# Optimization experiments

Measured on AMD Instinct MI355X. Metric: run time of the kernel, lower is better.

## Reference

```python
import jax, jax.numpy as jnp
import numpy as np

D_MODEL = 2048
NUM_HEADS = 16
D_KV = D_MODEL // NUM_HEADS
THETA = 10000.0
N_LORA = 4
RANK = 16
BATCH = 2
SEQ = 2048


def setup_inputs() -> dict:
    key = jax.random.key(0)
    ks = jax.random.split(key, 16)
    s = 0.02
    inp = {
        'x': jax.random.normal(ks[0], (BATCH, SEQ, D_MODEL), jnp.float32),
        'lora_start_indices': jnp.sort(jax.random.randint(ks[1], (N_LORA,), 0, BATCH)),
        'Wq': jax.random.normal(ks[2], (D_MODEL, D_MODEL), jnp.float32) * s,
        'Aq': jax.random.normal(ks[3], (N_LORA, RANK, D_MODEL), jnp.float32) * s,
        'Bq': jax.random.normal(ks[4], (N_LORA, D_MODEL, RANK), jnp.float32) * s,
        'Wk': jax.random.normal(ks[5], (D_MODEL, D_MODEL), jnp.float32) * s,
        'Ak': jax.random.normal(ks[6], (N_LORA, RANK, D_MODEL), jnp.float32) * s,
        'Bk': jax.random.normal(ks[7], (N_LORA, D_MODEL, RANK), jnp.float32) * s,
        'Wv': jax.random.normal(ks[8], (D_MODEL, D_MODEL), jnp.float32) * s,
        'Av': jax.random.normal(ks[9], (N_LORA, RANK, D_MODEL), jnp.float32) * s,
        'Bv': jax.random.normal(ks[10], (N_LORA, D_MODEL, RANK), jnp.float32) * s,
        'Wo': jax.random.normal(ks[11], (D_MODEL, D_MODEL), jnp.float32) * s,
        'Ao': jax.random.normal(ks[12], (N_LORA, RANK, D_MODEL), jnp.float32) * s,
        'Bo': jax.random.normal(ks[13], (N_LORA, D_MODEL, RANK), jnp.float32) * s,
    }
    return inp


def _adapter_ids(starts, batch):
    # each batch row b uses the adapter whose start index is the last one <= b
    ids = jnp.searchsorted(starts, jnp.arange(batch), side='right') - 1
    return jnp.clip(ids, 0, starts.shape[0] - 1)


def _multilora(x, ids, W, A, B):
    # x: [b, s, d_in]; W: [d_out, d_in]; A: [L, r, d_in]; B: [L, d_out, r]
    base = jnp.einsum('bsd,od->bso', x, W)
    Ai, Bi = A[ids], B[ids]                       # [b, r, d_in], [b, d_out, r]
    low = jnp.einsum('bsd,brd->bsr', x, Ai)
    return base + jnp.einsum('bsr,bor->bso', low, Bi)


def _rope(x):
    # x: [b, h, s, d]; interleaved pair rotation
    d = x.shape[-1]
    pos = jnp.arange(x.shape[-2], dtype=jnp.float32)
    inv_freq = THETA ** (-jnp.arange(0, d, 2, dtype=jnp.float32) / d)  # [d/2]
    ang = pos[:, None] * inv_freq[None, :]                              # [s, d/2]
    cos, sin = jnp.cos(ang), jnp.sin(ang)
    x1, x2 = x[..., 0::2], x[..., 1::2]
    o1 = x1 * cos - x2 * sin
    o2 = x1 * sin + x2 * cos
    return jnp.stack([o1, o2], axis=-1).reshape(x.shape)


def reference(x, lora_start_indices, Wq, Aq, Bq, Wk, Ak, Bk, Wv, Av, Bv, Wo, Ao, Bo):
    b, s, _ = x.shape
    ids = _adapter_ids(lora_start_indices, b)
    Q = _multilora(x, ids, Wq, Aq, Bq)
    K = _multilora(x, ids, Wk, Ak, Bk)
    V = _multilora(x, ids, Wv, Av, Bv)
    # [b, s, h*d] -> [b, h, s, d]
    split = lambda t: t.reshape(b, s, NUM_HEADS, D_KV).transpose(0, 2, 1, 3)
    Q, K, V = split(Q), split(K), split(V)
    Q, K = _rope(Q), _rope(K)
    scores = jnp.einsum('bhqd,bhkd->bhqk', Q, K) / jnp.sqrt(jnp.asarray(D_KV, x.dtype))
    causal = jnp.tril(jnp.ones((s, s), bool))
    scores = jnp.where(causal, scores, jnp.asarray(-jnp.inf, scores.dtype))
    attn = jax.nn.softmax(scores, axis=-1)
    out = jnp.einsum('bhqk,bhkd->bhqd', attn, V)
    out = out.transpose(0, 2, 1, 3).reshape(b, s, D_MODEL)
    return _multilora(out, ids, Wo, Ao, Bo)
```

## Files before the change

### kernel.cpp

```cpp
#include <hip/hip_runtime.h>

typedef unsigned short u16;
typedef unsigned int   u32;
typedef __bf16  bf16x8 __attribute__((ext_vector_type(8)));
typedef float   f32x4  __attribute__((ext_vector_type(4)));

#define D_MODEL 2048
#define SEQ     2048
#define NHEAD   16
#define DKV     128
#define RANK    16

__device__ __forceinline__ u16 f2b(float f) {
  union { float f; u32 i; } v; v.f = f;
  u32 i = v.i;
  return (u16)((i + 0x7FFFu + ((i >> 16) & 1u)) >> 16);
}
__device__ __forceinline__ u32 pack2(float lo, float hi) {
  return (u32)f2b(lo) | ((u32)f2b(hi) << 16);
}
__device__ __forceinline__ float b2f(u16 u) {
  union { u32 i; float f; } v; v.i = ((u32)u) << 16; return v.f;
}
__device__ __forceinline__ float dot2(u32 xa, u32 aa) {
  return b2f((u16)(xa & 0xFFFFu)) * b2f((u16)(aa & 0xFFFFu)) +
         b2f((u16)(xa >> 16))     * b2f((u16)(aa >> 16));
}
__device__ __forceinline__ int adapter_id(const int* starts, int b) {
  int cnt = 0;
#pragma unroll
  for (int i = 0; i < 4; ++i) cnt += (starts[i] <= b) ? 1 : 0;
  int id = cnt - 1;
  return id < 0 ? 0 : (id > 3 ? 3 : id);
}
__device__ __forceinline__ f32x4 mfma16(bf16x8 a, bf16x8 b, f32x4 c) {
  return __builtin_amdgcn_mfma_f32_16x16x32_bf16(a, b, c, 0, 0, 0);
}

struct CvtArgs {
  const float* src[13];
  u32 base[14];
};
__global__ __launch_bounds__(256) void k_convert(CvtArgs a, u16* __restrict__ dst) {
  const u32 c = blockIdx.x * 256 + threadIdx.x;
  const u32 el0 = c * 8;
  if (el0 >= a.base[13]) return;
  int t = 0;
#pragma unroll
  for (int i = 1; i < 13; ++i) t += (el0 >= a.base[i]) ? 1 : 0;
  const float* s = a.src[t] + (el0 - a.base[t]);
  const float4 lo = *(const float4*)s;
  const float4 hi = *(const float4*)(s + 4);
  uint4 r;
  r.x = pack2(lo.x, lo.y); r.y = pack2(lo.z, lo.w);
  r.z = pack2(hi.x, hi.y); r.w = pack2(hi.z, hi.w);
  *(uint4*)(dst + el0) = r;
}

template <int TAG>
__global__ __launch_bounds__(256) void k_lowrank(
    const u16* __restrict__ X, const u16* __restrict__ A0,
    const u16* __restrict__ A1, const u16* __restrict__ A2,
    const int* __restrict__ starts, float* __restrict__ low, int nout)
{
  const int m = blockIdx.x;
  const int w = threadIdx.x >> 6, lane = threadIdx.x & 63;
  const int id = adapter_id(starts, m >> 11);
  const u16* Xr = X + (size_t)m * D_MODEL;
  for (int o = w; o < nout; o += 4) {
    const int p = o >> 4, r = o & 15;
    const u16* Ar = (p == 0 ? A0 : p == 1 ? A1 : A2) + (size_t)(id * 16 + r) * D_MODEL;
    float sum = 0.f;
#pragma unroll
    for (int c = 0; c < 4; ++c) {
      const int d = c * 512 + lane * 8;
      const uint4 xv = *(const uint4*)(Xr + d);
      const uint4 av = *(const uint4*)(Ar + d);
      sum += dot2(xv.x, av.x) + dot2(xv.y, av.y) + dot2(xv.z, av.z) + dot2(xv.w, av.w);
    }
#pragma unroll
    for (int off = 32; off >= 1; off >>= 1) sum += __shfl_xor(sum, off, 64);
    if (lane == 0) low[(size_t)m * nout + o] = sum;
  }
}

template <int QKV>
__global__ __launch_bounds__(256, 2) void k_gemm(
    const u16* __restrict__ X,
    const u16* __restrict__ W0, const u16* __restrict__ W1, const u16* __restrict__ W2,
    const u16* __restrict__ B0, const u16* __restrict__ B1, const u16* __restrict__ B2,
    const float* __restrict__ low, int ldlow,
    const int* __restrict__ starts,
    u16* __restrict__ D0, u16* __restrict__ D1, u16* __restrict__ D2,
    float* __restrict__ Df)
{
  __shared__ __attribute__((aligned(16))) u16 At[128 * 32];
  __shared__ __attribute__((aligned(16))) u16 Bt[128 * 32];
  const int tid = threadIdx.x;
  const int w = tid >> 6, lane = tid & 63, quad = lane >> 4, l16 = lane & 15;
  const int wr = w >> 1, wc = w & 1;
  const int n0 = blockIdx.x * 128, m0 = blockIdx.y * 128, z = blockIdx.z;
  const u16* W  = (z == 0) ? W0 : (z == 1) ? W1 : W2;
  const u16* Bm = (z == 0) ? B0 : (z == 1) ? B1 : B2;
  u16*       D  = (z == 0) ? D0 : (z == 1) ? D1 : D2;
  const int loff = QKV ? z * RANK : 0;
  const int id = adapter_id(starts, m0 >> 11);

  const f32x4 zero4 = {0.f, 0.f, 0.f, 0.f};
  f32x4 acc[4][4];
#pragma unroll
  for (int i = 0; i < 4; ++i)
#pragma unroll
    for (int j = 0; j < 4; ++j) acc[i][j] = zero4;

  const int srow = tid >> 2;
  const int scol = (tid & 3) * 8;
  const u16* Xg = X + (size_t)(m0 + srow) * D_MODEL + scol;
  const u16* Wg = W + (size_t)(n0 + srow) * D_MODEL + scol;

  uint4 ra0 = *(const uint4*)(Xg);
  uint4 ra1 = *(const uint4*)(Xg + 64 * D_MODEL);
  uint4 rb0 = *(const uint4*)(Wg);
  uint4 rb1 = *(const uint4*)(Wg + 64 * D_MODEL);

  for (int kt = 0; kt < D_MODEL / 32; ++kt) {
    *(uint4*)(At + srow * 32 + scol)        = ra0;
    *(uint4*)(At + (64 + srow) * 32 + scol) = ra1;
    *(uint4*)(Bt + srow * 32 + scol)        = rb0;
    *(uint4*)(Bt + (64 + srow) * 32 + scol) = rb1;
    __syncthreads();
    if (kt < D_MODEL / 32 - 1) {
      const int kb = (kt + 1) * 32;
      ra0 = *(const uint4*)(Xg + kb);
      ra1 = *(const uint4*)(Xg + 64 * D_MODEL + kb);
      rb0 = *(const uint4*)(Wg + kb);
      rb1 = *(const uint4*)(Wg + 64 * D_MODEL + kb);
    }
    bf16x8 af[4], bfr[4];
#pragma unroll
    for (int i = 0; i < 4; ++i)
      af[i] = *(const bf16x8*)&At[(wr * 64 + i * 16 + l16) * 32 + quad * 8];
#pragma unroll
    for (int j = 0; j < 4; ++j)
      bfr[j] = *(const bf16x8*)&Bt[(wc * 64 + j * 16 + l16) * 32 + quad * 8];
#pragma unroll
    for (int i = 0; i < 4; ++i)
#pragma unroll
      for (int j = 0; j < 4; ++j)
        acc[i][j] = mfma16(af[i], bfr[j], acc[i][j]);
    __syncthreads();
  }

  for (int e = tid; e < 4096; e += 256) {
    const int rr = e >> 5, kk = e & 31;
    u16 av = 0, bv = 0;
    if (kk < RANK) {
      av = f2b(low[(size_t)(m0 + rr) * ldlow + loff + kk]);
      bv = Bm[((size_t)id * D_MODEL + n0 + rr) * RANK + kk];
    }
    At[rr * 32 + kk] = av;
    Bt[rr * 32 + kk] = bv;
  }
  __syncthreads();
  {
    bf16x8 af[4], bfr[4];
#pragma unroll
    for (int i = 0; i < 4; ++i)
      af[i] = *(const bf16x8*)&At[(wr * 64 + i * 16 + l16) * 32 + quad * 8];
#pragma unroll
    for (int j = 0; j < 4; ++j)
      bfr[j] = *(const bf16x8*)&Bt[(wc * 64 + j * 16 + l16) * 32 + quad * 8];
#pragma unroll
    for (int i = 0; i < 4; ++i)
#pragma unroll
      for (int j = 0; j < 4; ++j)
        acc[i][j] = mfma16(af[i], bfr[j], acc[i][j]);
  }

  if (QKV) {
    const float scale = (z == 0) ? 0.08838834764831845f : 1.0f;
    const int ropez = (z <= 1);
#pragma unroll
    for (int i = 0; i < 4; ++i) {
      const int mrow = m0 + wr * 64 + i * 16 + quad * 4;
#pragma unroll
      for (int j = 0; j < 4; ++j) {
        const int col = n0 + wc * 64 + j * 16 + l16;
        const int hh = col >> 7, jj = col & (DKV - 1);
        const float invf = exp2f(-0.20762050593046f * (float)(jj >> 1));
#pragma unroll
        for (int r = 0; r < 4; ++r) {
          const int m = mrow + r;
          const int bb = m >> 11, srw = m & (SEQ - 1);
          float v = acc[i][j][r] * scale;
          if (ropez) {
            float sn, cs;
            __sincosf((float)srw * invf, &sn, &cs);
            const float part = __shfl_xor(v, 1, 64);
            v = (jj & 1) ? (part * sn + v * cs) : (v * cs - part * sn);
          }
          D[(((size_t)(bb * NHEAD + hh)) * SEQ + srw) * DKV + jj] = f2b(v);
        }
      }
    }
  } else {
#pragma unroll
    for (int i = 0; i < 4; ++i) {
      const int mrow = m0 + wr * 64 + i * 16 + quad * 4;
#pragma unroll
      for (int j = 0; j < 4; ++j) {
        const int col = n0 + wc * 64 + j * 16 + l16;
#pragma unroll
        for (int r = 0; r < 4; ++r)
          Df[(size_t)(mrow + r) * D_MODEL + col] = acc[i][j][r];
      }
    }
  }
}

#define M0 8.0f
__global__ __launch_bounds__(256, 3) void k_flash(
    const u16* __restrict__ Q, const u16* __restrict__ K,
    const u16* __restrict__ V, u16* __restrict__ O,
    u16* __restrict__ Opart, float* __restrict__ lpart)
{
  __shared__ __attribute__((aligned(16))) u16 Kl[64 * 136];
  __shared__ __attribute__((aligned(16))) u16 VT[DKV * 72];
  __shared__ __attribute__((aligned(16))) u16 Pl[4 * 16 * 72];
  const int tid = threadIdx.x;
  const int w = tid >> 6, lane = tid & 63, quad = lane >> 4, l16 = lane & 15;
  const int cid = blockIdx.x, bh = blockIdx.y;
  const size_t base = (size_t)bh * SEQ * DKV;
  const u16* Qb = Q + base;
  const u16* Kb = K + base;
  const u16* Vb = V + base;
  const int b = bh >> 4, h = bh & 15;
  u16* Plw = &Pl[w * 1152];
  const f32x4 zero4 = {0.f, 0.f, 0.f, 0.f};

  const int dual = (cid < 16);
  const int nA   = dual ? (cid + 1) : 16;
  const int qtB  = 31 - cid;
  const int n    = dual ? 17 : 16;

  const int krr = tid >> 4;
  const int kc8 = (tid & 15) * 8;
  const int vrp = tid & 31;
  const int vcg = tid >> 5;

  int qt = cid, q0 = cid * 64;
  bf16x8 qa[4];
#pragma unroll
  for (int kc = 0; kc < 4; ++kc)
    qa[kc] = *(const bf16x8*)(Qb + (size_t)(q0 + w * 16 + l16) * DKV + kc * 32 + quad * 8);

  f32x4 oacc[8];
#pragma unroll
  for (int nn = 0; nn < 8; ++nn) oacc[nn] = zero4;
  float lr[4] = {0.f, 0.f, 0.f, 0.f};

  uint4 pk[4], pva[2], pvb[2];
#pragma unroll
  for (int it = 0; it < 4; ++it)
    pk[it] = *(const uint4*)(Kb + (size_t)(krr + it * 16) * DKV + kc8);
#pragma unroll
  for (int it = 0; it < 2; ++it) {
    pva[it] = *(const uint4*)(Vb + (size_t)(2 * vrp)     * DKV + (vcg + it * 8) * 8);
    pvb[it] = *(const uint4*)(Vb + (size_t)(2 * vrp + 1) * DKV + (vcg + it * 8) * 8);
  }

  for (int s = 0; s < n; ++s) {
    if (dual && s == nA) {
      float inv[4];
#pragma unroll
      for (int rg = 0; rg < 4; ++rg) {
        float t = lr[rg];
#pragma unroll
        for (int off = 8; off >= 1; off >>= 1) t += __shfl_xor(t, off, 64);
        inv[rg] = 1.f / t;
        lr[rg] = 0.f;
      }
#pragma unroll
      for (int nn = 0; nn < 8; ++nn) {
        const int col = h * DKV + nn * 16 + l16;
#pragma unroll
        for (int rg = 0; rg < 4; ++rg) {
          const int row = q0 + w * 16 + quad * 4 + rg;
          O[((size_t)b * SEQ + row) * D_MODEL + col] = f2b(oacc[nn][rg] * inv[rg]);
        }
#pragma unroll
        for (int e = 0; e < 4; ++e) oacc[nn][e] = 0.f;
      }
      qt = qtB; q0 = qtB * 64;
#pragma unroll
      for (int kc = 0; kc < 4; ++kc)
        qa[kc] = *(const bf16x8*)(Qb + (size_t)(q0 + w * 16 + l16) * DKV + kc * 32 + quad * 8);
    }
    const int kt = (dual && s >= nA) ? (16 + s - nA) : s;

    __syncthreads();
#pragma unroll
    for (int it = 0; it < 4; ++it)
      *(uint4*)(&Kl[(krr + it * 16) * 136 + kc8]) = pk[it];
#pragma unroll
    for (int it = 0; it < 2; ++it) {
      const int c0 = (vcg + it * 8) * 8;
      const uint4 a = pva[it], c = pvb[it];
      *(u32*)&VT[(c0 + 0) * 72 + 2 * vrp] = (a.x & 0xFFFFu) | (c.x << 16);
      *(u32*)&VT[(c0 + 1) * 72 + 2 * vrp] = (a.x >> 16)     | (c.x & 0xFFFF0000u);
      *(u32*)&VT[(c0 + 2) * 72 + 2 * vrp] = (a.y & 0xFFFFu) | (c.y << 16);
      *(u32*)&VT[(c0 + 3) * 72 + 2 * vrp] = (a.y >> 16)     | (c.y & 0xFFFF0000u);
      *(u32*)&VT[(c0 + 4) * 72 + 2 * vrp] = (a.z & 0xFFFFu) | (c.z << 16);
      *(u32*)&VT[(c0 + 5) * 72 + 2 * vrp] = (a.z >> 16)     | (c.z & 0xFFFF0000u);
      *(u32*)&VT[(c0 + 6) * 72 + 2 * vrp] = (a.w & 0xFFFFu) | (c.w << 16);
      *(u32*)&VT[(c0 + 7) * 72 + 2 * vrp] = (a.w >> 16)     | (c.w & 0xFFFF0000u);
    }
    __syncthreads();

    if (s + 1 < n) {
      const int ktn = (dual && (s + 1) >= nA) ? (16 + s + 1 - nA) : (s + 1);
      const size_t ko = (size_t)ktn * 64 * DKV;
#pragma unroll
      for (int it = 0; it < 4; ++it)
        pk[it] = *(const uint4*)(Kb + ko + (size_t)(krr + it * 16) * DKV + kc8);
#pragma unroll
      for (int it = 0; it < 2; ++it) {
        pva[it] = *(const uint4*)(Vb + ko + (size_t)(2 * vrp)     * DKV + (vcg + it * 8) * 8);
        pvb[it] = *(const uint4*)(Vb + ko + (size_t)(2 * vrp + 1) * DKV + (vcg + it * 8) * 8);
      }
    }

    f32x4 sacc[4];
#pragma unroll
    for (int jc = 0; jc < 4; ++jc) sacc[jc] = zero4;
#pragma unroll
    for (int kc = 0; kc < 4; ++kc)
#pragma unroll
      for (int jc = 0; jc < 4; ++jc) {
        const bf16x8 kb = *(const bf16x8*)&Kl[(jc * 16 + l16) * 136 + kc * 32 + quad * 8];
        sacc[jc] = mfma16(qa[kc], kb, sacc[jc]);
      }

    const int diag = (kt == qt);
#pragma unroll
    for (int rg = 0; rg < 4; ++rg) {
      const int qq = q0 + w * 16 + quad * 4 + rg;
      float psum = 0.f;
#pragma unroll
      for (int jc = 0; jc < 4; ++jc) {
        const int kk = kt * 64 + jc * 16 + l16;
        float p = __expf(sacc[jc][rg] - M0);
        if (diag && kk > qq) p = 0.f;
        psum += p;
        Plw[(quad * 4 + rg) * 72 + jc * 16 + l16] = f2b(p);
      }
      lr[rg] += psum;
    }

#pragma unroll
    for (int kc = 0; kc < 2; ++kc) {
      const bf16x8 pa = *(const bf16x8*)&Plw[l16 * 72 + kc * 32 + quad * 8];
#pragma unroll
      for (int nn = 0; nn < 8; ++nn) {
        const bf16x8 vb = *(const bf16x8*)&VT[(nn * 16 + l16) * 72 + kc * 32 + quad * 8];
        oacc[nn] = mfma16(pa, vb, oacc[nn]);
      }
    }
  }

  const int j = dual ? 1 : 0;
  const int slot = (bh * 16 + (qt - 16)) * 2 + j;
#pragma unroll
  for (int rg = 0; rg < 4; ++rg) {
#pragma unroll
    for (int off = 8; off >= 1; off >>= 1) lr[rg] += __shfl_xor(lr[rg], off, 64);
  }
#pragma unroll
  for (int nn = 0; nn < 8; ++nn) {
#pragma unroll
    for (int rg = 0; rg < 4; ++rg) {
      const int row = w * 16 + quad * 4 + rg;
      Opart[(size_t)slot * 8192 + row * 128 + nn * 16 + l16] = f2b(oacc[nn][rg]);
    }
  }
  if (l16 == 0) {
#pragma unroll
    for (int rg = 0; rg < 4; ++rg)
      lpart[slot * 64 + w * 16 + quad * 4 + rg] = lr[rg];
  }
}

__global__ __launch_bounds__(256) void k_merge(
    const u16* __restrict__ Opart, const float* __restrict__ lpart,
    u16* __restrict__ O)
{
  const u32 t = blockIdx.x * 256 + threadIdx.x;
  const u32 u   = t & 63;
  const u32 row = (t >> 6) & 63;
  const u32 q16 = (t >> 12) & 15;
  const u32 bh  = t >> 16;
  const u32 slot0 = (bh * 16 + q16) * 2;
  const u32 o0 = ((slot0 * 8192u + row * 128u) >> 1) + u;
  const u32 a = ((const u32*)Opart)[o0];
  const u32 c = ((const u32*)Opart)[o0 + 4096];
  const float inv = 1.f / (lpart[slot0 * 64 + row] + lpart[(slot0 + 1) * 64 + row]);
  const float r0 = (b2f((u16)(a & 0xFFFFu)) + b2f((u16)(c & 0xFFFFu))) * inv;
  const float r1 = (b2f((u16)(a >> 16))     + b2f((u16)(c >> 16)))     * inv;
  const u32 bb = bh >> 4, h = bh & 15;
  const u32 s = (q16 + 16) * 64 + row;
  ((u32*)O)[(size_t)(bb * SEQ + s) * (D_MODEL / 2) + h * 64 + u] = pack2(r0, r1);
}

extern "C" void kernel_launch(void* const* d_in, const int* in_sizes, int n_in,
                              void* d_out, int out_size, void* d_ws, size_t ws_size,
                              hipStream_t stream) {
  (void)in_sizes; (void)n_in; (void)out_size; (void)ws_size;
  const int* starts = (const int*)d_in[1];

  static const u32 XB = 0;
  static const u32 WQ = 8388608, WK = 12582912, WV = 16777216, WO = 20971520;
  static const u32 AQ = 25165824, AK = 25296896, AV = 25427968, AO = 25559040;
  static const u32 BQ = 25690112, BK = 25821184, BV = 25952256, BO = 26083328;
  static const u32 TOT = 26214400;

  u16* wsb = (u16*)d_ws;
  char* ws = (char*)d_ws;
  float* low_qkv = (float*)(ws + 52428800);
  float* low_o   = (float*)(ws + 53215232);
  u16*   Qb      = (u16*)(ws + 53477376);
  u16*   Kb      = (u16*)(ws + 70254592);
  u16*   Vb      = (u16*)(ws + 87031808);
  u16*   attn    = wsb + XB;
  u16*   Opart   = (u16*)d_out;
  float* lpart   = (float*)((char*)d_out + 16777216);

  CvtArgs ca;
  ca.src[0]  = (const float*)d_in[0];
  ca.src[1]  = (const float*)d_in[2];
  ca.src[2]  = (const float*)d_in[5];
  ca.src[3]  = (const float*)d_in[8];
  ca.src[4]  = (const float*)d_in[11];
  ca.src[5]  = (const float*)d_in[3];
  ca.src[6]  = (const float*)d_in[6];
  ca.src[7]  = (const float*)d_in[9];
  ca.src[8]  = (const float*)d_in[12];
  ca.src[9]  = (const float*)d_in[4];
  ca.src[10] = (const float*)d_in[7];
  ca.src[11] = (const float*)d_in[10];
  ca.src[12] = (const float*)d_in[13];
  const u32 bases[14] = {XB, WQ, WK, WV, WO, AQ, AK, AV, AO, BQ, BK, BV, BO, TOT};
  for (int i = 0; i < 14; ++i) ca.base[i] = bases[i];

  k_convert<<<dim3(TOT / 8 / 256), 256, 0, stream>>>(ca, wsb);

  k_lowrank<0><<<dim3(4096), 256, 0, stream>>>(wsb + XB, wsb + AQ, wsb + AK, wsb + AV,
                                               starts, low_qkv, 48);
  k_gemm<1><<<dim3(16, 32, 3), 256, 0, stream>>>(
      wsb + XB, wsb + WQ, wsb + WK, wsb + WV, wsb + BQ, wsb + BK, wsb + BV,
      low_qkv, 48, starts, Qb, Kb, Vb, (float*)nullptr);
  k_flash<<<dim3(32, 32), 256, 0, stream>>>(Qb, Kb, Vb, attn, Opart, lpart);
  k_merge<<<dim3(8192), 256, 0, stream>>>(Opart, lpart, attn);
  k_lowrank<1><<<dim3(4096), 256, 0, stream>>>(attn, wsb + AO, wsb + AO, wsb + AO,
                                               starts, low_o, 16);
  k_gemm<0><<<dim3(16, 32, 1), 256, 0, stream>>>(
      attn, wsb + WO, wsb + WO, wsb + WO, wsb + BO, wsb + BO, wsb + BO,
      low_o, 16, starts, (u16*)nullptr, (u16*)nullptr, (u16*)nullptr,
      (float*)d_out);
}
```

Before: 521.6 us.

## Load GEMM tiles directly into LDS and alias flash P buffer onto K tile

```diff
diff --git a/kernel.cpp b/kernel.cpp
--- a/kernel.cpp
+++ b/kernel.cpp
@@ -35,6 +35,11 @@
 }
 __device__ __forceinline__ f32x4 mfma16(bf16x8 a, bf16x8 b, f32x4 c) {
   return __builtin_amdgcn_mfma_f32_16x16x32_bf16(a, b, c, 0, 0, 0);
+}
+__device__ __forceinline__ void gload16(const u16* g, u16* l) {
+  __builtin_amdgcn_global_load_lds(
+      (const __attribute__((address_space(1))) u32*)(const void*)g,
+      (__attribute__((address_space(3))) u32*)(void*)l, 16, 0, 0);
 }
 
 struct CvtArgs {
@@ -117,25 +122,16 @@
   const int scol = (tid & 3) * 8;
   const u16* Xg = X + (size_t)(m0 + srow) * D_MODEL + scol;
   const u16* Wg = W + (size_t)(n0 + srow) * D_MODEL + scol;
-
-  uint4 ra0 = *(const uint4*)(Xg);
-  uint4 ra1 = *(const uint4*)(Xg + 64 * D_MODEL);
-  uint4 rb0 = *(const uint4*)(Wg);
-  uint4 rb1 = *(const uint4*)(Wg + 64 * D_MODEL);
+  u16* lA = &At[w * 512];
+  u16* lB = &Bt[w * 512];
 
   for (int kt = 0; kt < D_MODEL / 32; ++kt) {
-    *(uint4*)(At + srow * 32 + scol)        = ra0;
-    *(uint4*)(At + (64 + srow) * 32 + scol) = ra1;
-    *(uint4*)(Bt + srow * 32 + scol)        = rb0;
-    *(uint4*)(Bt + (64 + srow) * 32 + scol) = rb1;
+    const int kb = kt * 32;
+    gload16(Xg + kb,                lA);
+    gload16(Xg + 64 * D_MODEL + kb, lA + 2048);
+    gload16(Wg + kb,                lB);
+    gload16(Wg + 64 * D_MODEL + kb, lB + 2048);
     __syncthreads();
-    if (kt < D_MODEL / 32 - 1) {
-      const int kb = (kt + 1) * 32;
-      ra0 = *(const uint4*)(Xg + kb);
-      ra1 = *(const uint4*)(Xg + 64 * D_MODEL + kb);
-      rb0 = *(const uint4*)(Wg + kb);
-      rb1 = *(const uint4*)(Wg + 64 * D_MODEL + kb);
-    }
     bf16x8 af[4], bfr[4];
 #pragma unroll
     for (int i = 0; i < 4; ++i)
@@ -219,14 +215,13 @@
 }
 
 #define M0 8.0f
-__global__ __launch_bounds__(256, 3) void k_flash(
+__global__ __launch_bounds__(256, 4) void k_flash(
     const u16* __restrict__ Q, const u16* __restrict__ K,
     const u16* __restrict__ V, u16* __restrict__ O,
     u16* __restrict__ Opart, float* __restrict__ lpart)
 {
   __shared__ __attribute__((aligned(16))) u16 Kl[64 * 136];
   __shared__ __attribute__((aligned(16))) u16 VT[DKV * 72];
-  __shared__ __attribute__((aligned(16))) u16 Pl[4 * 16 * 72];
   const int tid = threadIdx.x;
   const int w = tid >> 6, lane = tid & 63, quad = lane >> 4, l16 = lane & 15;
   const int cid = blockIdx.x, bh = blockIdx.y;
@@ -235,7 +230,7 @@
   const u16* Kb = K + base;
   const u16* Vb = V + base;
   const int b = bh >> 4, h = bh & 15;
-  u16* Plw = &Pl[w * 1152];
+  u16* Plw = &Kl[w * 1152];
   const f32x4 zero4 = {0.f, 0.f, 0.f, 0.f};
 
   const int dual = (cid < 16);
@@ -351,11 +346,18 @@
         const int kk = kt * 64 + jc * 16 + l16;
         float p = __expf(sacc[jc][rg] - M0);
         if (diag && kk > qq) p = 0.f;
+        sacc[jc][rg] = p;
         psum += p;
-        Plw[(quad * 4 + rg) * 72 + jc * 16 + l16] = f2b(p);
       }
       lr[rg] += psum;
     }
+
+    __syncthreads();
+#pragma unroll
+    for (int rg = 0; rg < 4; ++rg)
+#pragma unroll
+      for (int jc = 0; jc < 4; ++jc)
+        Plw[(quad * 4 + rg) * 72 + jc * 16 + l16] = f2b(sacc[jc][rg]);
 
 #pragma unroll
     for (int kc = 0; kc < 2; ++kc) {
```

New measurement: 523.7 us. No clear change (+0.4%).
